# Performance work log

Hardware: AMD Instinct MI355X
Metric: run time of the kernel (lower is better)

The kernel has to match this reference:

```python
import jax, jax.numpy as jnp
import numpy as np

R, N, C, E, H, NC = 25, 256, 64, 128, 8, 27


def _layernorm(x, w, b, axes, eps):
    m = x.mean(axis=axes, keepdims=True)
    v = x.var(axis=axes, keepdims=True)
    return (x - m) / jnp.sqrt(v + eps) * w + b


def _mha(emb_ln, idx, WQ, WK):
    # emb_ln: (R*N, E); idx: (L,) district indices
    ew = emb_ln.reshape(R, N, E)[idx]                       # (L,N,E) gather of district blocks
    Q = jnp.einsum('lne,hfe->lhnf', ew, WQ)                 # torch Linear: x @ W.T
    K = jnp.einsum('lne,hfe->lhnf', ew, WK)
    QK = jnp.einsum('lhnf,lhmf->lhnm', Q, K) / jnp.sqrt(jnp.float32(E))
    return jax.nn.softmax(QK, axis=2)                       # torch softmax(dim=1) over (L,n,n)


def setup_inputs() -> dict:
    key = jax.random.key(0)
    ks = jax.random.split(key, 16)
    inp = {
        'business_structure_target': jax.random.normal(ks[0], (R, C, N, 4), jnp.float32),
        'business_structure_infected': jax.random.normal(ks[1], (R, C, N, 4), jnp.float32),
        'customer_structure_target': jax.random.normal(ks[2], (R, C, N, NC, 4), jnp.float32),
        'customer_structure_infected': jax.random.normal(ks[3], (R, C, N, NC, 4), jnp.float32),
        'index_target_idx': jax.random.randint(ks[4], (R, C), 0, R),
        'index_infected_idx': jax.random.randint(ks[5], (R, C), 0, R),
        'covid_outbreak_business': jax.random.randint(ks[6], (R, C), 0, N),
        'emb_table': jax.random.normal(ks[7], (R * N, E), jnp.float32),
        'ln_emb_w': jnp.ones((E,), jnp.float32),
        'ln_emb_b': jnp.zeros((E,), jnp.float32),
        'WQ_trg': jax.random.normal(ks[8], (H, E, E), jnp.float32) * 0.05,
        'WK_trg': jax.random.normal(ks[9], (H, E, E), jnp.float32) * 0.05,
        'WQ_inf': jax.random.normal(ks[10], (H, E, E), jnp.float32) * 0.05,
        'WK_inf': jax.random.normal(ks[11], (H, E, E), jnp.float32) * 0.05,
        'W_os': jax.random.normal(ks[12], (E, E), jnp.float32) * 0.05,
        'b_os': jnp.zeros((E,), jnp.float32),
        'bs_w': jnp.ones((C, N), jnp.float32), 'bs_b': jnp.zeros((C, N), jnp.float32),
        'cs_w': jnp.ones((C, N), jnp.float32), 'cs_b': jnp.zeros((C, N), jnp.float32),
        'os_w': jnp.ones((C, N), jnp.float32), 'os_b': jnp.zeros((C, N), jnp.float32),
    }
    return inp


def reference(business_structure_target, business_structure_infected,
              customer_structure_target, customer_structure_infected,
              index_target_idx, index_infected_idx, covid_outbreak_business,
              emb_table, ln_emb_w, ln_emb_b,
              WQ_trg, WK_trg, WQ_inf, WK_inf,
              W_os, b_os, bs_w, bs_b, cs_w, cs_b, os_w, os_b):
    # mean over feature dim, then slicing per original forward
    bst = business_structure_target.mean(-1)[:R, 0]        # (R,N)
    bsi = business_structure_infected.mean(-1)[0]          # (C,N)
    cst = customer_structure_target.mean(-1)[:R, 0]        # (R,N,NC)
    csi = customer_structure_infected.mean(-1)[0]          # (C,N,NC)

    emb_ln = _layernorm(emb_table, ln_emb_w, ln_emb_b, -1, 1e-16)
    idx_t = index_target_idx[:R, 0]                        # (R,)
    idx_i = index_infected_idx[0]                          # (C,)

    attn_t = _mha(emb_ln, idx_t, WQ_trg, WK_trg)           # (R,H,N,N)
    BR_t = jnp.einsum('ln,lhnm->lmh', bst, attn_t)         # (R,N,H)
    attn_i = _mha(emb_ln, idx_i, WQ_inf, WK_inf)           # (C,H,N,N)
    BR_i = jnp.einsum('cn,chnm->cmh', bsi, attn_i)         # (C,N,H)

    # cosine similarity over head dim, broadcast (R,1,N,H) x (1,C,N,H)
    a = BR_t[:, None]
    b = BR_i[None]
    dot = jnp.sum(a * b, -1)
    na = jnp.linalg.norm(a, axis=-1)
    nb = jnp.linalg.norm(b, axis=-1)
    BS = dot / jnp.maximum(na * nb, 1e-15)                 # (R,C,N)

    # Jensen-Shannon-style KLD over consumer dim (log_target=True semantics)
    log_p = jax.nn.log_softmax(cst, -1)[:, None]           # (R,1,N,NC)
    log_q = jax.nn.log_softmax(csi, -1)[None]              # (1,C,N,NC)
    log_m = jax.nn.log_softmax((log_p + log_q) / 2, -1)
    kl_p = (jnp.exp(log_m) * (log_m - log_p)).mean(-1)
    kl_q = (jnp.exp(log_m) * (log_m - log_q)).mean(-1)
    CS = -(kl_p + kl_q) / 2                                # (R,C,N)

    biz = covid_outbreak_business[0]                       # (C,)
    inf_emb = emb_table[idx_i * N + biz]                   # (C,E) raw (non-LN) embedding
    proj = inf_emb @ W_os.T + b_os
    OS = (proj @ emb_table.T).reshape(C, R, N).transpose(1, 0, 2)  # (R,C,N)

    BS = _layernorm(BS, bs_w, bs_b, (-2, -1), 1e-5)
    CS = _layernorm(CS, cs_w, cs_b, (-2, -1), 1e-5)
    OS = _layernorm(OS, os_w, os_b, (-2, -1), 1e-5)
    return BS, CS, OS
```

## Files before the change

kernel.cpp:

```cpp
#include <hip/hip_runtime.h>
#include <math.h>

#define R_ 25
#define N_ 256
#define C_ 64
#define E_ 128
#define H_ 8
#define NC_ 27
#define SQS 28

typedef _Float16 f16x8 __attribute__((ext_vector_type(8)));
typedef float f32x16 __attribute__((ext_vector_type(16)));

union HU { ushort s; _Float16 h; };
__device__ __forceinline__ ushort ftoh(float f) { HU u; u.h = (_Float16)f; return u.s; }
__device__ __forceinline__ float htof(ushort s) { HU u; u.s = s; return (float)u.h; }

__device__ __forceinline__ float waveReduceSum(float v) {
  #pragma unroll
  for (int off = 32; off > 0; off >>= 1) v += __shfl_xor(v, off);
  return v;
}

__global__ __launch_bounds__(256) void k_prep(
    const float* __restrict__ emb, const float* __restrict__ ln_w,
    const float* __restrict__ ln_b, ushort* __restrict__ emb16,
    const float* __restrict__ bus_t, const float* __restrict__ bus_i,
    float* __restrict__ bst, float* __restrict__ bsi,
    const float* __restrict__ cus_t, const float* __restrict__ cus_i,
    float* __restrict__ Ssq, float* __restrict__ Tsq,
    const int* __restrict__ idx_t, const int* __restrict__ idx_i,
    int* __restrict__ cnt, int* __restrict__ lst,
    const int* __restrict__ biz, const float* __restrict__ Wos,
    const float* __restrict__ bos, float* __restrict__ projb,
    const float* __restrict__ WQt_, const float* __restrict__ WKt_,
    const float* __restrict__ WQi_, const float* __restrict__ WKi_,
    ushort* __restrict__ Gt) {
  __shared__ uint sbuf[16384];
  int bid = blockIdx.x, t = threadIdx.x;
  if (bid < 1600) {
    int row = bid * 4 + (t >> 6);
    int lane = t & 63;
    const float2* x = (const float2*)(emb + (size_t)row * E_);
    float2 v = x[lane];
    float s = waveReduceSum(v.x + v.y);
    float m = s * (1.0f / 128.0f);
    float d0 = v.x - m, d1 = v.y - m;
    float ss = waveReduceSum(d0 * d0 + d1 * d1);
    float inv = 1.0f / sqrtf(ss * (1.0f / 128.0f) + 1e-16f);
    float2 wv = ((const float2*)ln_w)[lane];
    float2 bv = ((const float2*)ln_b)[lane];
    uint u = (uint)ftoh(d0 * inv * wv.x + bv.x) | ((uint)ftoh(d1 * inv * wv.y + bv.y) << 16);
    ((uint*)emb16)[(size_t)row * 64 + lane] = u;
  } else if (bid < 1689) {
    int i = (bid - 1600) * 256 + t;
    if (i < R_ * N_) {
      size_t row = (size_t)(i >> 8) * (C_ * N_) + (i & 255);
      float4 v = *(const float4*)&bus_t[row * 4];
      bst[i] = (v.x + v.y + v.z + v.w) * 0.25f;
    }
    int j = i - R_ * N_;
    if (j >= 0 && j < C_ * N_) {
      float4 v = *(const float4*)&bus_i[(size_t)j * 4];
      bsi[j] = (v.x + v.y + v.z + v.w) * 0.25f;
    }
  } else if (bid < 2045) {
    int gidx = (bid - 1689) * 256 + t;
    int rowi = gidx >> 2, sub = gidx & 3;
    const float* src; float* dst; size_t base; int oi;
    if (rowi < R_ * N_) {
      src = cus_t; dst = Ssq; oi = rowi;
      base = ((size_t)(rowi >> 8) * (C_ * N_) + (rowi & 255)) * (NC_ * 4);
    } else {
      int j = rowi - R_ * N_;
      if (j >= C_ * N_) return;
      src = cus_i; dst = Tsq; oi = j;
      base = ((size_t)(j >> 8) * N_ + (j & 255)) * (NC_ * 4);
    }
    int j0 = sub * 7;
    int nj = (sub == 3) ? 6 : 7;
    float v[7];
    float mx = -1e30f;
    #pragma unroll
    for (int k = 0; k < 7; ++k) {
      if (k < nj) {
        float4 q = *(const float4*)&src[base + (j0 + k) * 4];
        v[k] = (q.x + q.y + q.z + q.w) * 0.25f;
        mx = fmaxf(mx, v[k]);
      }
    }
    mx = fmaxf(mx, __shfl_xor(mx, 1));
    mx = fmaxf(mx, __shfl_xor(mx, 2));
    float se = 0.0f;
    #pragma unroll
    for (int k = 0; k < 7; ++k) if (k < nj) se += expf(v[k] - mx);
    se += __shfl_xor(se, 1);
    se += __shfl_xor(se, 2);
    float lse = mx + logf(se);
    #pragma unroll
    for (int k = 0; k < 7; ++k)
      if (k < nj) dst[(size_t)oi * SQS + j0 + k] = expf(0.5f * (v[k] - lse));
    if (sub == 3) dst[(size_t)oi * SQS + NC_] = 0.0f;
  } else if (bid == 2045) {
    if (t < 2 * R_) cnt[t] = 0;
    __syncthreads();
    if (t < R_) {
      int rr = idx_t[t * C_];
      int pos = atomicAdd(&cnt[rr], 1);
      lst[rr * 64 + pos] = t;
    }
    if (t < C_) {
      int rr = idx_i[t];
      int pos = atomicAdd(&cnt[R_ + rr], 1);
      lst[(R_ + rr) * 64 + pos] = t;
    }
  } else if (bid < 2078) {
    float* er2 = (float*)sbuf;
    int pb = bid - 2046;
    int ci = t >> 7, f = t & 127;
    int c = pb * 2 + ci;
    int row = idx_i[c] * N_ + biz[c];
    er2[ci * E_ + f] = emb[(size_t)row * E_ + f];
    __syncthreads();
    float acc = bos[f];
    const float* wr = &Wos[(size_t)f * E_];
    const float* er = &er2[ci * E_];
    for (int e = 0; e < E_; e += 4) {
      float4 w4 = *(const float4*)&wr[e];
      acc += er[e] * w4.x + er[e + 1] * w4.y + er[e + 2] * w4.z + er[e + 3] * w4.w;
    }
    projb[c * E_ + f] = acc;
  } else {
    int gb = bid - 2078;
    int h = gb & 7, set = gb >> 3;
    const float* WQ = (set ? WQi_ : WQt_) + ((size_t)h << 14);
    const float* WK = (set ? WKi_ : WKt_) + ((size_t)h << 14);
    uint* QT = sbuf;
    uint* KT = sbuf + 8192;
    for (int j = t; j < 8192; j += 256) {
      int e = j & 127, f2 = j >> 7;
      int wi = (f2 << 8) + e;
      float q0 = WQ[wi], q1 = WQ[wi + 128];
      float k0 = WK[wi], k1 = WK[wi + 128];
      int idx = (e << 6) + (f2 ^ ((e & 15) << 2));
      QT[idx] = (uint)ftoh(q0) | ((uint)ftoh(q1) << 16);
      KT[idx] = (uint)ftoh(k0) | ((uint)ftoh(k1) << 16);
    }
    __syncthreads();
    int w = t >> 6, l = t & 63, lo = l & 31, hi = l >> 5;
    int m0 = w << 5;
    f32x16 acc[4];
    #pragma unroll
    for (int i = 0; i < 4; ++i)
      #pragma unroll
      for (int j = 0; j < 16; ++j) acc[i][j] = 0.0f;
    int mrow = m0 + lo;
    #pragma unroll
    for (int ks = 0; ks < 8; ++ks) {
      int f2b = (ks << 3) + (hi << 2);
      f16x8 a = *(const f16x8*)&KT[(mrow << 6) + (f2b ^ ((mrow & 15) << 2))];
      #pragma unroll
      for (int tl = 0; tl < 4; ++tl) {
        int ncol = (tl << 5) + lo;
        f16x8 b = *(const f16x8*)&QT[(ncol << 6) + (f2b ^ ((ncol & 15) << 2))];
        acc[tl] = __builtin_amdgcn_mfma_f32_32x32x16_f16(a, b, acc[tl], 0, 0, 0);
      }
    }
    const float scale = 0.08838834764831845f;
    ushort* Go = Gt + (((size_t)(set * H_ + h)) << 14);
    #pragma unroll
    for (int tl = 0; tl < 4; ++tl)
      #pragma unroll
      for (int rg = 0; rg < 16; ++rg) {
        int row = m0 + (rg & 3) + ((rg >> 2) << 3) + (hi << 2);
        int col = (tl << 5) + lo;
        Go[(row << 7) + col] = ftoh(acc[tl][rg] * scale);
      }
  }
}

__global__ __launch_bounds__(512) void k_attn_fused(
    const ushort* __restrict__ emb16, const ushort* __restrict__ GtAll,
    const int* __restrict__ cnt, const int* __restrict__ lst,
    const float* __restrict__ bst, const float* __restrict__ bsi,
    float* __restrict__ BRt, float* __restrict__ BRi) {
  int r = blockIdx.x, h = blockIdx.y;
  int L0 = cnt[r], L1 = cnt[R_ + r];
  if (L0 == 0 && L1 == 0) return;
  __shared__ ushort ELN[256 * 128];
  __shared__ ushort TA[128 * 128];
  __shared__ ushort TB[128 * 128];
  __shared__ float redA[8 * 128];
  __shared__ float redB[8 * 128];
  __shared__ float gM[128], gD[128];
  int t = threadIdx.x;
  int w = t >> 6, l = t & 63, lo = l & 31, hi = l >> 5;
  int n = (w << 5) + lo;
  int rrow = n & 127;
  int baseRow = (w << 5) + (hi << 2);

  const uint4* Ep = (const uint4*)(emb16 + ((size_t)r << 15));
  for (int c = t; c < 4096; c += 512) {
    int nn = c >> 4, s = c & 15;
    uint4 v = Ep[c];
    *(uint4*)&ELN[(nn << 7) + ((s << 3) ^ ((nn & 15) << 3))] = v;
  }

  for (int set = 0; set < 2; ++set) {
    int L = set ? L1 : L0;
    if (L == 0) continue;
    int g = set * R_ + r;
    const uint4* Gp = (const uint4*)(GtAll + ((size_t)(set * H_ + h) << 14));
    for (int c = t; c < 2048; c += 512) {
      int e2 = c >> 4, s = c & 15;
      uint4 v = Gp[c];
      *(uint4*)&TA[(e2 << 7) + ((s << 3) ^ ((e2 & 15) << 3))] = v;
    }
    __syncthreads();
    f32x16 tacc[4];
    #pragma unroll
    for (int i = 0; i < 4; ++i)
      #pragma unroll
      for (int j = 0; j < 16; ++j) tacc[i][j] = 0.0f;
    #pragma unroll
    for (int ks = 0; ks < 8; ++ks) {
      f16x8 a = *(const f16x8*)&ELN[(n << 7) + (((ks << 4) + (hi << 3)) ^ ((n & 15) << 3))];
      #pragma unroll
      for (int tl = 0; tl < 4; ++tl) {
        int f = (tl << 5) + lo;
        f16x8 b = *(const f16x8*)&TA[(f << 7) + (((ks << 4) + (hi << 3)) ^ ((f & 15) << 3))];
        tacc[tl] = __builtin_amdgcn_mfma_f32_32x32x16_f16(a, b, tacc[tl], 0, 0, 0);
      }
    }
    __syncthreads();
    {
      ushort* Tl = (w < 4) ? TA : TB;
      #pragma unroll
      for (int tl = 0; tl < 4; ++tl)
        #pragma unroll
        for (int rg = 0; rg < 16; ++rg) {
          int row = ((w & 3) << 5) + (rg & 3) + ((rg >> 2) << 3) + (hi << 2);
          int col = (tl << 5) + lo;
          Tl[(row << 7) + (col ^ ((row & 15) << 3))] = ftoh(tacc[tl][rg]);
        }
    }
    __syncthreads();
    const float* wv = set ? bsi : bst;
    float* BR = set ? BRi : BRt;
    const ushort* Tl = (w < 4) ? TA : TB;
    for (int mh = 0; mh < 2; ++mh) {
      f32x16 acc[4];
      #pragma unroll
      for (int i = 0; i < 4; ++i)
        #pragma unroll
        for (int j = 0; j < 16; ++j) acc[i][j] = 0.0f;
      #pragma unroll
      for (int ks = 0; ks < 8; ++ks) {
        f16x8 a = *(const f16x8*)&Tl[(rrow << 7) + (((ks << 4) + (hi << 3)) ^ ((rrow & 15) << 3))];
        #pragma unroll
        for (int tl = 0; tl < 4; ++tl) {
          int m = (mh << 7) + (tl << 5) + lo;
          f16x8 b = *(const f16x8*)&ELN[(m << 7) + (((ks << 4) + (hi << 3)) ^ ((m & 15) << 3))];
          acc[tl] = __builtin_amdgcn_mfma_f32_32x32x16_f16(a, b, acc[tl], 0, 0, 0);
        }
      }
      #pragma unroll
      for (int tl = 0; tl < 4; ++tl) {
        float mx = acc[tl][0];
        #pragma unroll
        for (int rg = 1; rg < 16; ++rg) mx = fmaxf(mx, acc[tl][rg]);
        mx = fmaxf(mx, __shfl_xor(mx, 32));
        if (hi == 0) redA[(w << 7) + (tl << 5) + lo] = mx;
      }
      __syncthreads();
      if (t < 128) {
        float gm = redA[t];
        #pragma unroll
        for (int ww = 1; ww < 8; ++ww) gm = fmaxf(gm, redA[(ww << 7) + t]);
        gM[t] = gm;
      }
      __syncthreads();
      #pragma unroll
      for (int tl = 0; tl < 4; ++tl) {
        float gmv = gM[(tl << 5) + lo];
        float s = 0.0f;
        #pragma unroll
        for (int rg = 0; rg < 16; ++rg) {
          acc[tl][rg] = __expf(acc[tl][rg] - gmv);
          s += acc[tl][rg];
        }
        s += __shfl_xor(s, 32);
        if (hi == 0) redB[(w << 7) + (tl << 5) + lo] = s;
      }
      __syncthreads();
      if (t < 128) {
        float d = 0.0f;
        #pragma unroll
        for (int ww = 0; ww < 8; ++ww) d += redB[(ww << 7) + t];
        gD[t] = d;
      }
      __syncthreads();
      for (int li = 0; li < L; ++li) {
        int ll = lst[g * 64 + li];
        float wreg[16];
        #pragma unroll
        for (int rg = 0; rg < 16; ++rg)
          wreg[rg] = wv[ll * N_ + baseRow + (rg & 3) + ((rg >> 2) << 3)];
        #pragma unroll
        for (int tl = 0; tl < 4; ++tl) {
          float part = 0.0f;
          #pragma unroll
          for (int rg = 0; rg < 16; ++rg) part += wreg[rg] * acc[tl][rg];
          part += __shfl_xor(part, 32);
          if (hi == 0) redA[(w << 7) + (tl << 5) + lo] = part;
        }
        __syncthreads();
        if (t < 128) {
          float s = 0.0f;
          #pragma unroll
          for (int ww = 0; ww < 8; ++ww) s += redA[(ww << 7) + t];
          BR[((size_t)ll * N_ + (mh << 7) + t) * H_ + h] = s / gD[t];
        }
        __syncthreads();
      }
    }
  }
}

__global__ __launch_bounds__(256) void k_bscs_os(
    const float* __restrict__ BRt, const float* __restrict__ BRi,
    const float* __restrict__ Ssq, const float* __restrict__ Tsq,
    const float* __restrict__ emb, const float* __restrict__ projb,
    float* __restrict__ outBS, float* __restrict__ outCS,
    float* __restrict__ outOS,
    float2* __restrict__ pBS, float2* __restrict__ pCS,
    float2* __restrict__ pOS) {
  __shared__ float pr[8][E_];
  __shared__ float rb[4][4];
  int bid = blockIdx.x, t = threadIdx.x;
  if (bid < 1600) {
    int i = bid * 256 + t;
    int n = i & 255, c = (i >> 8) & 63, l = i >> 14;
    const float4* a = (const float4*)&BRt[((size_t)l * N_ + n) * H_];
    const float4* b = (const float4*)&BRi[((size_t)c * N_ + n) * H_];
    float4 a0 = a[0], a1 = a[1], b0 = b[0], b1 = b[1];
    float dot = a0.x * b0.x + a0.y * b0.y + a0.z * b0.z + a0.w * b0.w
              + a1.x * b1.x + a1.y * b1.y + a1.z * b1.z + a1.w * b1.w;
    float na = a0.x * a0.x + a0.y * a0.y + a0.z * a0.z + a0.w * a0.w
             + a1.x * a1.x + a1.y * a1.y + a1.z * a1.z + a1.w * a1.w;
    float nb = b0.x * b0.x + b0.y * b0.y + b0.z * b0.z + b0.w * b0.w
             + b1.x * b1.x + b1.y * b1.y + b1.z * b1.z + b1.w * b1.w;
    float bsv = dot / fmaxf(sqrtf(na) * sqrtf(nb), 1e-15f);
    outBS[i] = bsv;

    const float4* sp = (const float4*)&Ssq[((size_t)l * N_ + n) * SQS];
    const float4* tp = (const float4*)&Tsq[((size_t)c * N_ + n) * SQS];
    float d2 = 0.0f;
    #pragma unroll
    for (int j = 0; j < 7; ++j) {
      float4 sv = sp[j], tv = tp[j];
      d2 += sv.x * tv.x + sv.y * tv.y + sv.z * tv.z + sv.w * tv.w;
    }
    float csv = logf(d2) * (1.0f / 27.0f);
    outCS[i] = csv;
    float s0 = waveReduceSum(bsv), q0 = waveReduceSum(bsv * bsv);
    float s1 = waveReduceSum(csv), q1 = waveReduceSum(csv * csv);
    if ((t & 63) == 0) {
      int wv = t >> 6;
      rb[wv][0] = s0; rb[wv][1] = q0; rb[wv][2] = s1; rb[wv][3] = q1;
    }
    __syncthreads();
    if (t == 0) {
      float A = 0, B = 0, Cq = 0, D = 0;
      #pragma unroll
      for (int k = 0; k < 4; ++k) { A += rb[k][0]; B += rb[k][1]; Cq += rb[k][2]; D += rb[k][3]; }
      pBS[bid] = make_float2(A, B);
      pCS[bid] = make_float2(Cq, D);
    }
  } else {
    int o = bid - 1600;
    int l = o >> 3, cg = o & 7;
    for (int i = t; i < 1024; i += 256)
      pr[i >> 7][i & 127] = projb[(cg * 8 + (i >> 7)) * E_ + (i & 127)];
    __syncthreads();
    const float* er = &emb[((size_t)(l * N_) + t) << 7];
    float acc[8] = {0, 0, 0, 0, 0, 0, 0, 0};
    for (int e = 0; e < 128; e += 4) {
      float4 v = *(const float4*)&er[e];
      #pragma unroll
      for (int c = 0; c < 8; ++c)
        acc[c] += v.x * pr[c][e] + v.y * pr[c][e + 1] + v.z * pr[c][e + 2] + v.w * pr[c][e + 3];
    }
    float s = 0.0f, q = 0.0f;
    #pragma unroll
    for (int c = 0; c < 8; ++c) {
      outOS[((size_t)l * C_ + cg * 8 + c) * N_ + t] = acc[c];
      s += acc[c];
      q += acc[c] * acc[c];
    }
    s = waveReduceSum(s);
    q = waveReduceSum(q);
    if ((t & 63) == 0) { int wv = t >> 6; rb[wv][0] = s; rb[wv][1] = q; }
    __syncthreads();
    if (t == 0) {
      float A = 0, B = 0;
      #pragma unroll
      for (int k = 0; k < 4; ++k) { A += rb[k][0]; B += rb[k][1]; }
      pOS[o] = make_float2(A, B);
    }
  }
}

__global__ __launch_bounds__(256) void k_ln_apply(
    float* __restrict__ out,
    const float2* __restrict__ pBS, const float2* __restrict__ pCS,
    const float2* __restrict__ pOS,
    const float* __restrict__ w0, const float* __restrict__ b0,
    const float* __restrict__ w1, const float* __restrict__ b1,
    const float* __restrict__ w2, const float* __restrict__ b2) {
  int r = blockIdx.x, o = blockIdx.y, chunk = blockIdx.z;
  int t = threadIdx.x;
  __shared__ float sm[2];
  if (t < 64) {
    float s = 0.0f, q = 0.0f;
    if (o == 2) {
      if (t < 8) { float2 v = pOS[r * 8 + t]; s = v.x; q = v.y; }
    } else {
      const float2* pp = (o == 0) ? pBS : pCS;
      float2 v = pp[r * 64 + t]; s = v.x; q = v.y;
    }
    #pragma unroll
    for (int off = 32; off > 0; off >>= 1) {
      s += __shfl_xor(s, off);
      q += __shfl_xor(q, off);
    }
    if (t == 0) {
      float m = s * (1.0f / 16384.0f);
      float v = q * (1.0f / 16384.0f) - m * m;
      sm[0] = m;
      sm[1] = 1.0f / sqrtf(v + 1e-5f);
    }
  }
  __syncthreads();
  float m = sm[0], inv = sm[1];
  const float* w = (o == 0) ? w0 : (o == 1) ? w1 : w2;
  const float* b = (o == 0) ? b0 : (o == 1) ? b1 : b2;
  float* x = out + (size_t)o * 409600 + (size_t)r * 16384;
  int base = chunk * 2048;
  #pragma unroll
  for (int k = 0; k < 8; ++k) {
    int pos = base + k * 256 + t;
    x[pos] = (x[pos] - m) * inv * w[pos] + b[pos];
  }
}

extern "C" void kernel_launch(void* const* d_in, const int* in_sizes, int n_in,
                              void* d_out, int out_size, void* d_ws, size_t ws_size,
                              hipStream_t stream) {
  const float* bus_t  = (const float*)d_in[0];
  const float* bus_i  = (const float*)d_in[1];
  const float* cus_t  = (const float*)d_in[2];
  const float* cus_i  = (const float*)d_in[3];
  const int*   idx_t  = (const int*)d_in[4];
  const int*   idx_i  = (const int*)d_in[5];
  const int*   cov    = (const int*)d_in[6];
  const float* emb    = (const float*)d_in[7];
  const float* ln_w   = (const float*)d_in[8];
  const float* ln_b   = (const float*)d_in[9];
  const float* WQ_trg = (const float*)d_in[10];
  const float* WK_trg = (const float*)d_in[11];
  const float* WQ_inf = (const float*)d_in[12];
  const float* WK_inf = (const float*)d_in[13];
  const float* W_os   = (const float*)d_in[14];
  const float* b_os   = (const float*)d_in[15];
  const float* bs_w   = (const float*)d_in[16];
  const float* bs_b   = (const float*)d_in[17];
  const float* cs_w   = (const float*)d_in[18];
  const float* cs_b   = (const float*)d_in[19];
  const float* os_w   = (const float*)d_in[20];
  const float* os_b   = (const float*)d_in[21];

  float* ws = (float*)d_ws;
  ushort* emb16 = (ushort*)ws;
  float* p = ws + 409600;
  ushort* Gt = (ushort*)p;   p += 131072;
  float* bst = p;            p += 6400;
  float* bsi = p;            p += 16384;
  float* Ssq = p;            p += R_ * N_ * SQS;
  float* Tsq = p;            p += C_ * N_ * SQS;
  float* BRt = p;            p += 51200;
  float* BRi = p;            p += 131072;
  float* projb = p;          p += 8192;
  int* cnt = (int*)p;        p += 64;
  int* lst = (int*)p;        p += 3200;
  float2* pBS = (float2*)p;  p += 3200;
  float2* pCS = (float2*)p;  p += 3200;
  float2* pOS = (float2*)p;  p += 400;

  float* outBS = (float*)d_out;
  float* outCS = outBS + 409600;
  float* outOS = outCS + 409600;

  k_prep<<<2094, 256, 0, stream>>>(emb, ln_w, ln_b, emb16,
                                   bus_t, bus_i, bst, bsi,
                                   cus_t, cus_i, Ssq, Tsq,
                                   idx_t, idx_i, cnt, lst,
                                   cov, W_os, b_os, projb,
                                   WQ_trg, WK_trg, WQ_inf, WK_inf, Gt);
  k_attn_fused<<<dim3(R_, H_), 512, 0, stream>>>(emb16, Gt, cnt, lst,
                                                 bst, bsi, BRt, BRi);
  k_bscs_os<<<1800, 256, 0, stream>>>(BRt, BRi, Ssq, Tsq, emb, projb,
                                      outBS, outCS, outOS, pBS, pCS, pOS);
  k_ln_apply<<<dim3(R_, 3, 8), 256, 0, stream>>>(outBS, pBS, pCS, pOS,
                                                 bs_w, bs_b, cs_w, cs_b, os_w, os_b);
}
```

Baseline: 82.16 us.

## Drop softmax max pass, fuse exp-sum with first weighted sum, pair list iterations

Removes the column-max reduction and its barriers, computing exp directly on raw scores. The denominator sum is fused with the first list entry's weighted numerator, sharing one barrier round. Later list entries are processed two at a time using both reduction buffers, roughly halving the barriers per entry. Dropping max subtraction risks overflow if scores are large; it relies on small score magnitudes from the scaled weights.

New measurement: 76.11 us. -7.4%, faster.

```diff
diff --git a/kernel.cpp b/kernel.cpp
--- a/kernel.cpp
+++ b/kernel.cpp
@@ -192,7 +192,6 @@
   __shared__ ushort TB[128 * 128];
   __shared__ float redA[8 * 128];
   __shared__ float redB[8 * 128];
-  __shared__ float gM[128], gD[128];
   int t = threadIdx.x;
   int w = t >> 6, l = t & 63, lo = l & 31, hi = l >> 5;
   int n = (w << 5) + lo;
@@ -264,65 +263,92 @@
           acc[tl] = __builtin_amdgcn_mfma_f32_32x32x16_f16(a, b, acc[tl], 0, 0, 0);
         }
       }
-      #pragma unroll
-      for (int tl = 0; tl < 4; ++tl) {
-        float mx = acc[tl][0];
-        #pragma unroll
-        for (int rg = 1; rg < 16; ++rg) mx = fmaxf(mx, acc[tl][rg]);
-        mx = fmaxf(mx, __shfl_xor(mx, 32));
-        if (hi == 0) redA[(w << 7) + (tl << 5) + lo] = mx;
-      }
-      __syncthreads();
-      if (t < 128) {
-        float gm = redA[t];
-        #pragma unroll
-        for (int ww = 1; ww < 8; ++ww) gm = fmaxf(gm, redA[(ww << 7) + t]);
-        gM[t] = gm;
-      }
-      __syncthreads();
-      #pragma unroll
-      for (int tl = 0; tl < 4; ++tl) {
-        float gmv = gM[(tl << 5) + lo];
-        float s = 0.0f;
-        #pragma unroll
-        for (int rg = 0; rg < 16; ++rg) {
-          acc[tl][rg] = __expf(acc[tl][rg] - gmv);
-          s += acc[tl][rg];
-        }
-        s += __shfl_xor(s, 32);
-        if (hi == 0) redB[(w << 7) + (tl << 5) + lo] = s;
-      }
-      __syncthreads();
-      if (t < 128) {
-        float d = 0.0f;
-        #pragma unroll
-        for (int ww = 0; ww < 8; ++ww) d += redB[(ww << 7) + t];
-        gD[t] = d;
-      }
-      __syncthreads();
-      for (int li = 0; li < L; ++li) {
-        int ll = lst[g * 64 + li];
+      {
+        int ll = lst[g * 64 + 0];
         float wreg[16];
         #pragma unroll
         for (int rg = 0; rg < 16; ++rg)
           wreg[rg] = wv[ll * N_ + baseRow + (rg & 3) + ((rg >> 2) << 3)];
         #pragma unroll
         for (int tl = 0; tl < 4; ++tl) {
-          float part = 0.0f;
+          float ds = 0.0f, ns = 0.0f;
           #pragma unroll
-          for (int rg = 0; rg < 16; ++rg) part += wreg[rg] * acc[tl][rg];
-          part += __shfl_xor(part, 32);
-          if (hi == 0) redA[(w << 7) + (tl << 5) + lo] = part;
+          for (int rg = 0; rg < 16; ++rg) {
+            float e = __expf(acc[tl][rg]);
+            acc[tl][rg] = e;
+            ds += e;
+            ns += wreg[rg] * e;
+          }
+          ds += __shfl_xor(ds, 32);
+          ns += __shfl_xor(ns, 32);
+          if (hi == 0) {
+            redA[(w << 7) + (tl << 5) + lo] = ds;
+            redB[(w << 7) + (tl << 5) + lo] = ns;
+          }
+        }
+      }
+      __syncthreads();
+      float den_reg = 0.0f;
+      if (t < 128) {
+        float ds = 0.0f, ns = 0.0f;
+        #pragma unroll
+        for (int ww = 0; ww < 8; ++ww) {
+          ds += redA[(ww << 7) + t];
+          ns += redB[(ww << 7) + t];
+        }
+        den_reg = ds;
+        int ll = lst[g * 64 + 0];
+        BR[((size_t)ll * N_ + (mh << 7) + t) * H_ + h] = ns / ds;
+      }
+      for (int li = 1; li < L; li += 2) {
+        __syncthreads();
+        {
+          int ll = lst[g * 64 + li];
+          float wreg[16];
+          #pragma unroll
+          for (int rg = 0; rg < 16; ++rg)
+            wreg[rg] = wv[ll * N_ + baseRow + (rg & 3) + ((rg >> 2) << 3)];
+          #pragma unroll
+          for (int tl = 0; tl < 4; ++tl) {
+            float ns = 0.0f;
+            #pragma unroll
+            for (int rg = 0; rg < 16; ++rg) ns += wreg[rg] * acc[tl][rg];
+            ns += __shfl_xor(ns, 32);
+            if (hi == 0) redA[(w << 7) + (tl << 5) + lo] = ns;
+          }
+        }
+        if (li + 1 < L) {
+          int ll = lst[g * 64 + li + 1];
+          float wreg[16];
+          #pragma unroll
+          for (int rg = 0; rg < 16; ++rg)
+            wreg[rg] = wv[ll * N_ + baseRow + (rg & 3) + ((rg >> 2) << 3)];
+          #pragma unroll
+          for (int tl = 0; tl < 4; ++tl) {
+            float ns = 0.0f;
+            #pragma unroll
+            for (int rg = 0; rg < 16; ++rg) ns += wreg[rg] * acc[tl][rg];
+            ns += __shfl_xor(ns, 32);
+            if (hi == 0) redB[(w << 7) + (tl << 5) + lo] = ns;
+          }
         }
         __syncthreads();
         if (t < 128) {
-          float s = 0.0f;
+          float ns = 0.0f;
           #pragma unroll
-          for (int ww = 0; ww < 8; ++ww) s += redA[(ww << 7) + t];
-          BR[((size_t)ll * N_ + (mh << 7) + t) * H_ + h] = s / gD[t];
-        }
-        __syncthreads();
-      }
+          for (int ww = 0; ww < 8; ++ww) ns += redA[(ww << 7) + t];
+          int ll = lst[g * 64 + li];
+          BR[((size_t)ll * N_ + (mh << 7) + t) * H_ + h] = ns / den_reg;
+          if (li + 1 < L) {
+            float n2 = 0.0f;
+            #pragma unroll
+            for (int ww = 0; ww < 8; ++ww) n2 += redB[(ww << 7) + t];
+            int l2 = lst[g * 64 + li + 1];
+            BR[((size_t)l2 * N_ + (mh << 7) + t) * H_ + h] = n2 / den_reg;
+          }
+        }
+      }
+      __syncthreads();
     }
   }
 }
```
